# Kernel tuning notes

Measured on AMD Instinct MI355X. Metric: run time of the kernel, lower is better.

The kernel has to match this reference:

```python
import jax, jax.numpy as jnp
import numpy as np

N = 50000        # nodes
E = 800000       # edges
F_IN = 128       # dataset.num_features (== dim*heads so all conv layers share in_channels)
DIM = 32         # mParams['dim']
HEADS = 4        # mParams['num_heads']
HC = DIM * HEADS # 128
DEPTH = 2        # mParams['c_depth'] -> total conv layers = DEPTH + 1 = 3
L = DEPTH + 1
DIM2 = 16        # ceil(DIM/2)
NCLS = 6
SLOPE = 0.2      # GATv2Conv default negative_slope


def setup_inputs() -> dict:
    key = jax.random.key(0)
    ks = jax.random.split(key, 20)
    def lin(k, fan_in, shape):
        return jax.random.normal(k, shape, dtype=jnp.float32) / np.sqrt(fan_in)
    x = jax.random.normal(ks[0], (N, F_IN), dtype=jnp.float32)
    edge_index = jax.random.randint(ks[1], (2, E), 0, N, dtype=jnp.int64)
    batch = jnp.zeros((N,), dtype=jnp.int64)
    # stacked GATv2Conv params (all layers have in_channels = 128)
    Wl = lin(ks[2], F_IN, (L, F_IN, HC))   # lin_l weight (source transform)
    Wr = lin(ks[3], F_IN, (L, F_IN, HC))   # lin_r weight (target transform)
    bl = jnp.zeros((L, HC), dtype=jnp.float32)
    br = jnp.zeros((L, HC), dtype=jnp.float32)
    att = lin(ks[4], DIM, (L, HEADS, DIM)) # attention vector a
    cb = jnp.zeros((L, HC), dtype=jnp.float32)  # conv output bias
    W1 = lin(ks[5], HC, (HC, DIM));   b1 = jnp.zeros((DIM,), jnp.float32)
    W2 = lin(ks[6], DIM, (DIM, DIM2)); b2 = jnp.zeros((DIM2,), jnp.float32)
    W3 = lin(ks[7], 2 * DIM2, (2 * DIM2, NCLS)); b3 = jnp.zeros((NCLS,), jnp.float32)
    return {"x": x, "edge_index": edge_index, "batch": batch,
            "Wl": Wl, "Wr": Wr, "bl": bl, "br": br, "att": att, "cb": cb,
            "W1": W1, "b1": b1, "W2": W2, "b2": b2, "W3": W3, "b3": b3}


def _gatv2_layer(h, src, dst, Wl, Wr, bl, br, att, cb):
    # h: [N, F]; src/dst: [Ea] (self-loops included)
    xl = (h @ Wl + bl).reshape(N, HEADS, DIM)  # source-side transform
    xr = (h @ Wr + br).reshape(N, HEADS, DIM)  # target-side transform
    msg = xl[src] + xr[dst]                    # [Ea, H, C]
    e = jnp.where(msg > 0, msg, SLOPE * msg)   # leaky_relu
    score = jnp.einsum('ehc,hc->eh', e, att)   # [Ea, H]
    # scatter-softmax over destination nodes
    m = jax.ops.segment_max(score, dst, num_segments=N)        # [N, H]
    ex = jnp.exp(score - m[dst])
    s = jax.ops.segment_sum(ex, dst, num_segments=N)           # [N, H]
    alpha = ex / (s[dst] + 1e-16)                              # [Ea, H]
    out = jax.ops.segment_sum(alpha[:, :, None] * xl[src], dst, num_segments=N)
    return out.reshape(N, HC) + cb


def reference(x, edge_index, batch, Wl, Wr, bl, br, att, cb, W1, b1, W2, b2, W3, b3):
    src0, dst0 = edge_index[0], edge_index[1]
    loop = jnp.arange(N, dtype=edge_index.dtype)
    src = jnp.concatenate([src0, loop])  # GATv2Conv add_self_loops=True
    dst = jnp.concatenate([dst0, loop])
    h = x
    for i in range(L):
        h = jax.nn.relu(_gatv2_layer(h, src, dst, Wl[i], Wr[i], bl[i], br[i], att[i], cb[i]))
    h = jax.nn.relu(h @ W1 + b1)
    h = jax.nn.relu(h @ W2 + b2)
    # dropout(p=0.5) is identity in eval mode
    e = jnp.concatenate([h[src0], h[dst0]], axis=1)  # [E, 2*DIM2]
    out = e @ W3 + b3                                # [E, NCLS]
    return (out, e)
```

## Files before the change

### kernel.cpp

```cpp
#include <hip/hip_runtime.h>
#include <hip/hip_bf16.h>

typedef __hip_bfloat16 bf16;
typedef __attribute__((ext_vector_type(8))) short bf16x8;
typedef __attribute__((ext_vector_type(4))) float f32x4;

#define N_NODES 50000
#define E_EDGES 800000
#define EA (E_EDGES + N_NODES)
#define HC 128
#define HEADS 4
#define DIM 32
#define DIM2 16
#define NCLS 6
#define SLOPE 0.2f
#define XN (N_NODES * HC)
#define GM 32
#define HSTRIDE 152
#define WSWZ_L 32768
#define NCHUNK ((N_NODES + 1023) / 1024)

#define P_CVTI (2 * E_EDGES)
#define P_PRM  6390
#define P_WSWZ (3 * WSWZ_L)
#define P_TOT  (P_CVTI + P_PRM + P_WSWZ)

__device__ __forceinline__ float b2f(bf16 v) { return __bfloat162float(v); }
__device__ __forceinline__ unsigned short f2bfu(float f) {
    bf16 b = __float2bfloat16(f);
    return *(unsigned short*)&b;
}
__device__ __forceinline__ unsigned packbf(float a, float b) {
    return (unsigned)f2bfu(a) | ((unsigned)f2bfu(b) << 16);
}

__device__ __forceinline__ void block_detect(const void* wptr, const void* eptr,
                                             int* det, int& isf32, int& is64) {
    int tid = threadIdx.x;
    if (tid == 0) { det[0] = 0; det[1] = 0; }
    __syncthreads();
    const unsigned short* w = (const unsigned short*)wptr;
    int badf = 0;
    for (int i = tid; i < 1024; i += 256) {
        unsigned v = w[i];
        unsigned ex = (v >> 7) & 0xFF;
        if (v != 0 && (ex < 90 || ex > 150)) badf++;
    }
    const int* ei = (const int*)eptr;
    int nz = 0;
    for (int i = tid; i < 1024; i += 256) {
        if (ei[2 * i + 1] != 0) nz++;
    }
    if (badf) atomicAdd(&det[0], badf);
    if (nz)   atomicAdd(&det[1], nz);
    __syncthreads();
    isf32 = det[0] > 100;
    is64  = det[1] < 100;
}

__global__ __launch_bounds__(256) void k_prep(
        const void* eraw, const void* sWl, const void* sWr,
        const void* sbl, const void* sbr, const void* satt, const void* scb,
        const void* sW1, const void* sb1, const void* sW2, const void* sb2,
        const void* sW3, const void* sb3,
        int* __restrict__ eidx, int* __restrict__ off,
        float* __restrict__ prm, unsigned short* __restrict__ wswz) {
    __shared__ int det[2];
    int isf32, is64;
    block_detect(sWl, eraw, det, isf32, is64);

    int i = blockIdx.x * 256 + threadIdx.x;
    if (i < P_CVTI) {
        int v = is64 ? (int)((const long long*)eraw)[i] : ((const int*)eraw)[i];
        if (v < 0) v = 0;
        if (v >= N_NODES) v = N_NODES - 1;
        eidx[i] = v;
        if (i >= E_EDGES) atomicAdd(&off[v], 1);
        return;
    }
    i -= P_CVTI;
    if (i < P_PRM) {
        int j = i + 98304;
        const void* src; float* dst; int o;
        if      (j < 98688)  { src = sbl;  dst = prm + 98304;  o = j - 98304; }
        else if (j < 99072)  { src = sbr;  dst = prm + 98688;  o = j - 98688; }
        else if (j < 99456)  { src = satt; dst = prm + 99072;  o = j - 99072; }
        else if (j < 99840)  { src = scb;  dst = prm + 99456;  o = j - 99456; }
        else if (j < 103936) { src = sW1;  dst = prm + 99840;  o = j - 99840; }
        else if (j < 103968) { src = sb1;  dst = prm + 103936; o = j - 103936; }
        else if (j < 104480) { src = sW2;  dst = prm + 103968; o = j - 103968; }
        else if (j < 104496) { src = sb2;  dst = prm + 104480; o = j - 104480; }
        else if (j < 104688) { src = sW3;  dst = prm + 104496; o = j - 104496; }
        else                 { src = sb3;  dst = prm + 104688; o = j - 104688; }
        dst[o] = isf32 ? ((const float*)src)[o] : b2f(((const bf16*)src)[o]);
        return;
    }
    i -= P_PRM;
    if (i >= P_WSWZ) return;
    int L = i / WSWZ_L;
    int e = i % WSWZ_L;
    int ntile = e >> 11;
    int r2 = e & 2047;
    int ks = r2 >> 9;
    int r3 = r2 & 511;
    int lane = r3 >> 3;
    int j = r3 & 7;
    int col = ntile * 16 + (lane & 15);
    int k = ks * 32 + (lane >> 4) * 8 + j;
    const void* src = (col < HC) ? sWl : sWr;
    int idx = L * HC * HC + k * HC + (col & (HC - 1));
    float v = isf32 ? ((const float*)src)[idx] : b2f(((const bf16*)src)[idx]);
    wswz[i] = f2bfu(v);
}

__global__ __launch_bounds__(1024) void k_scan1(int* __restrict__ off, int* __restrict__ part) {
    __shared__ int s[1024];
    int tid = threadIdx.x;
    int i = blockIdx.x * 1024 + tid;
    int v = (i < N_NODES) ? off[i] + 1 : 0;
    s[tid] = v;
    __syncthreads();
    for (int o = 1; o < 1024; o <<= 1) {
        int t = (tid >= o) ? s[tid - o] : 0;
        __syncthreads();
        s[tid] += t;
        __syncthreads();
    }
    if (i < N_NODES) off[i] = s[tid] - v;
    if (tid == 1023) part[blockIdx.x] = s[1023];
}

__global__ __launch_bounds__(64) void k_scan2(int* __restrict__ part) {
    int tid = threadIdx.x;
    int v = (tid < NCHUNK) ? part[tid] : 0;
    int orig = v;
    for (int o = 1; o < 64; o <<= 1) {
        int t = __shfl_up(v, o);
        if (tid >= o) v += t;
    }
    if (tid < NCHUNK) part[tid] = v - orig;
}

__global__ __launch_bounds__(1024) void k_scan3(int* __restrict__ off, const int* __restrict__ part) {
    int i = blockIdx.x * 1024 + threadIdx.x;
    if (i < N_NODES) off[i] += part[blockIdx.x];
    if (i == 0) off[N_NODES] = EA;
}

__global__ void k_scatter(const int* __restrict__ eidx, const int* __restrict__ off,
                          int* __restrict__ fill, int* __restrict__ csrsrc) {
    int e = blockIdx.x * blockDim.x + threadIdx.x;
    if (e >= EA) return;
    int src, dst;
    if (e < E_EDGES) { src = eidx[e]; dst = eidx[E_EDGES + e]; }
    else             { src = dst = e - E_EDGES; }
    int pos = off[dst] + atomicAdd(&fill[dst], 1);
    if (pos >= 0 && pos < EA) csrsrc[pos] = src;
}

__global__ __launch_bounds__(256) void k_gemm_mfma(
        const void* __restrict__ hsrc, const void* wdet, const void* edet,
        int detect_in,
        const unsigned short* __restrict__ wswz,
        const float* __restrict__ bl, const float* __restrict__ br,
        unsigned* __restrict__ xlbf, float* __restrict__ xr) {
    __shared__ unsigned short hs[GM * HSTRIDE];
    __shared__ int det[2];
    int tid = threadIdx.x;
    int wave = tid >> 6, lane = tid & 63;
    long row0 = (long)blockIdx.x * GM;

    int f32in = 0;
    if (detect_in) {
        int is64d;
        block_detect(wdet, edet, det, f32in, is64d);
    }

    if (f32in) {
        for (int idx = tid; idx < GM * 64; idx += 256) {
            int r = idx >> 6, cp = idx & 63;
            float v0 = 0.f, v1 = 0.f;
            if (row0 + r < N_NODES) {
                const float2 hv = ((const float2*)((const float*)hsrc + (row0 + r) * HC))[cp];
                v0 = hv.x; v1 = hv.y;
            }
            *(unsigned*)&hs[r * HSTRIDE + cp * 2] = packbf(v0, v1);
        }
    } else {
        for (int idx = tid; idx < GM * 64; idx += 256) {
            int r = idx >> 6, cp = idx & 63;
            unsigned u = 0;
            if (row0 + r < N_NODES)
                u = ((const unsigned*)hsrc)[(row0 + r) * (HC / 2) + cp];
            *(unsigned*)&hs[r * HSTRIDE + cp * 2] = u;
        }
    }
    __syncthreads();

    int q = lane >> 4, l16 = lane & 15;
    for (int nt = 0; nt < 4; nt++) {
        int colbase = wave * 64 + nt * 16;
        int col = colbase + l16;
        int ntile = colbase >> 4;
        f32x4 acc0 = {0.f, 0.f, 0.f, 0.f};
        f32x4 acc1 = {0.f, 0.f, 0.f, 0.f};
#pragma unroll
        for (int ks = 0; ks < 4; ks++) {
            bf16x8 bfrag = *(const bf16x8*)(wswz + (((ntile * 4 + ks) * 64 + lane) << 3));
            bf16x8 a0 = *(const bf16x8*)(hs + l16 * HSTRIDE + ks * 32 + q * 8);
            bf16x8 a1 = *(const bf16x8*)(hs + (16 + l16) * HSTRIDE + ks * 32 + q * 8);
            acc0 = __builtin_amdgcn_mfma_f32_16x16x32_bf16(a0, bfrag, acc0, 0, 0, 0);
            acc1 = __builtin_amdgcn_mfma_f32_16x16x32_bf16(a1, bfrag, acc1, 0, 0, 0);
        }
        if (col < HC) {
            float bias = bl[col];
#pragma unroll
            for (int reg = 0; reg < 4; reg++) {
                float v0 = acc0[reg] + bias;
                float v1 = acc1[reg] + bias;
                float p0 = __shfl_xor(v0, 1);
                float p1 = __shfl_xor(v1, 1);
                if ((lane & 1) == 0) {
                    long n0 = row0 + q * 4 + reg;
                    long n1 = row0 + 16 + q * 4 + reg;
                    unsigned u0 = packbf(v0, p0);
                    unsigned u1 = packbf(v1, p1);
                    int cp = col >> 1;
                    if (n0 < N_NODES) xlbf[n0 * (HC / 2) + cp] = u0;
                    if (n1 < N_NODES) xlbf[n1 * (HC / 2) + cp] = u1;
                }
            }
        } else {
            int c = col - HC;
            float bias = br[c];
#pragma unroll
            for (int reg = 0; reg < 4; reg++) {
                long n0 = row0 + q * 4 + reg;
                long n1 = row0 + 16 + q * 4 + reg;
                if (n0 < N_NODES) xr[n0 * HC + c] = acc0[reg] + bias;
                if (n1 < N_NODES) xr[n1 * HC + c] = acc1[reg] + bias;
            }
        }
    }
}

__global__ __launch_bounds__(256) void k_attn(
        const unsigned* __restrict__ xlbf, const float* __restrict__ xr,
        const int* __restrict__ off, const int* __restrict__ csrsrc,
        const float* __restrict__ att, const float* __restrict__ cb,
        void* __restrict__ hout, int out_bf16) {
    int wave = threadIdx.x >> 6;
    int lane = threadIdx.x & 63;
    int node = blockIdx.x * 4 + wave;
    if (node >= N_NODES) return;
    int grp = lane >> 4;
    int gl  = lane & 15;
    int fb  = gl * 8;
    int head = fb >> 5;

    const float4* xrp = (const float4*)(xr + (long)node * HC + fb);
    float4 xa = xrp[0], xb = xrp[1];
    const float4* ap = (const float4*)(att + head * DIM + (fb & 31));
    float4 aa = ap[0], ab = ap[1];

    int e0 = off[node], e1 = off[node + 1];
    if (e0 < 0) e0 = 0;
    if (e1 > EA) e1 = EA;
    if (e1 <= e0) {
        if (grp == 0) {
            if (out_bf16) {
                uint4 z = {0u, 0u, 0u, 0u};
                *(uint4*)((unsigned*)hout + (long)node * (HC / 2) + gl * 4) = z;
            } else {
                float4 z = make_float4(0.f, 0.f, 0.f, 0.f);
                ((float4*)((float*)hout + (long)node * HC + fb))[0] = z;
                ((float4*)((float*)hout + (long)node * HC + fb))[1] = z;
            }
        }
        return;
    }
    int klast = e1 - 1;

    int k0 = e0 + grp;
    int ka = k0 < klast ? k0 : klast;
    int kb = (k0 + 4) < klast ? (k0 + 4) : klast;
    int sa = csrsrc[ka];
    int sb = csrsrc[kb];
    uint4 u0 = ((const uint4*)(xlbf + (long)sa * (HC / 2)))[gl];
    uint4 u1 = ((const uint4*)(xlbf + (long)sb * (HC / 2)))[gl];

    float m = -1e30f, ssum = 0.f;
    float acc[8];
#pragma unroll
    for (int j = 0; j < 8; j++) acc[j] = 0.f;

    for (int kk = k0; kk < e1; kk += 4) {
        uint4 cur = u0;
        u0 = u1;
        int kp = (kk + 8) < klast ? (kk + 8) : klast;
        int sp = csrsrc[kp];
        u1 = ((const uint4*)(xlbf + (long)sp * (HC / 2)))[gl];

        float x0 = __uint_as_float(cur.x << 16);
        float x1 = __uint_as_float(cur.x & 0xffff0000u);
        float x2 = __uint_as_float(cur.y << 16);
        float x3 = __uint_as_float(cur.y & 0xffff0000u);
        float x4 = __uint_as_float(cur.z << 16);
        float x5 = __uint_as_float(cur.z & 0xffff0000u);
        float x6 = __uint_as_float(cur.w << 16);
        float x7 = __uint_as_float(cur.w & 0xffff0000u);
        float m0 = x0 + xa.x, m1 = x1 + xa.y, m2 = x2 + xa.z, m3 = x3 + xa.w;
        float m4 = x4 + xb.x, m5 = x5 + xb.y, m6 = x6 + xb.z, m7 = x7 + xb.w;
        float l0 = fmaxf(m0, SLOPE * m0), l1 = fmaxf(m1, SLOPE * m1);
        float l2 = fmaxf(m2, SLOPE * m2), l3 = fmaxf(m3, SLOPE * m3);
        float l4 = fmaxf(m4, SLOPE * m4), l5 = fmaxf(m5, SLOPE * m5);
        float l6 = fmaxf(m6, SLOPE * m6), l7 = fmaxf(m7, SLOPE * m7);
        float p = l0 * aa.x + l1 * aa.y + l2 * aa.z + l3 * aa.w
                + l4 * ab.x + l5 * ab.y + l6 * ab.z + l7 * ab.w;
        p += __shfl_xor(p, 1);
        p += __shfl_xor(p, 2);
        float mn = fmaxf(m, p);
        float sc = __expf(m - mn);
        float ex = __expf(p - mn);
        ssum = ssum * sc + ex;
        acc[0] = acc[0] * sc + ex * x0;
        acc[1] = acc[1] * sc + ex * x1;
        acc[2] = acc[2] * sc + ex * x2;
        acc[3] = acc[3] * sc + ex * x3;
        acc[4] = acc[4] * sc + ex * x4;
        acc[5] = acc[5] * sc + ex * x5;
        acc[6] = acc[6] * sc + ex * x6;
        acc[7] = acc[7] * sc + ex * x7;
        m = mn;
    }

#pragma unroll
    for (int d = 16; d <= 32; d <<= 1) {
        float mo = __shfl_xor(m, d);
        float so = __shfl_xor(ssum, d);
        float ao[8];
#pragma unroll
        for (int j = 0; j < 8; j++) ao[j] = __shfl_xor(acc[j], d);
        float mn = fmaxf(m, mo);
        float s1 = __expf(m - mn);
        float s2 = __expf(mo - mn);
        ssum = ssum * s1 + so * s2;
#pragma unroll
        for (int j = 0; j < 8; j++) acc[j] = acc[j] * s1 + ao[j] * s2;
        m = mn;
    }

    if (grp == 0) {
        float inv = 1.f / (ssum + 1e-16f);
        const float4* cbp = (const float4*)(cb + fb);
        float4 c0 = cbp[0], c1 = cbp[1];
        float o0 = fmaxf(acc[0] * inv + c0.x, 0.f);
        float o1 = fmaxf(acc[1] * inv + c0.y, 0.f);
        float o2 = fmaxf(acc[2] * inv + c0.z, 0.f);
        float o3 = fmaxf(acc[3] * inv + c0.w, 0.f);
        float o4 = fmaxf(acc[4] * inv + c1.x, 0.f);
        float o5 = fmaxf(acc[5] * inv + c1.y, 0.f);
        float o6 = fmaxf(acc[6] * inv + c1.z, 0.f);
        float o7 = fmaxf(acc[7] * inv + c1.w, 0.f);
        if (out_bf16) {
            uint4 w;
            w.x = packbf(o0, o1);
            w.y = packbf(o2, o3);
            w.z = packbf(o4, o5);
            w.w = packbf(o6, o7);
            *(uint4*)((unsigned*)hout + (long)node * (HC / 2) + gl * 4) = w;
        } else {
            float4 a0 = make_float4(o0, o1, o2, o3);
            float4 a1 = make_float4(o4, o5, o6, o7);
            float4* op = (float4*)((float*)hout + (long)node * HC + fb);
            op[0] = a0;
            op[1] = a1;
        }
    }
}

__global__ __launch_bounds__(256) void k_mlp(
        const float* __restrict__ h, const float* __restrict__ W1,
        const float* __restrict__ b1, const float* __restrict__ W2,
        const float* __restrict__ b2, float* __restrict__ h3) {
    __shared__ float w1s[HC * DIM];
    __shared__ float hs[16 * HC];
    __shared__ float h2s[16 * DIM];
    __shared__ float w2s[DIM * DIM2];
    int tid = threadIdx.x;
    long row0 = (long)blockIdx.x * 16;
    for (int idx = tid; idx < HC * DIM; idx += 256) w1s[idx] = W1[idx];
    for (int idx = tid; idx < DIM * DIM2; idx += 256) w2s[idx] = W2[idx];
    for (int idx = tid; idx < 16 * HC; idx += 256) {
        long g = row0 * HC + idx;
        hs[idx] = (g < (long)N_NODES * HC) ? h[g] : 0.f;
    }
    __syncthreads();
#pragma unroll
    for (int p = 0; p < 2; p++) {
        int idx = tid + p * 256;
        int r = idx >> 5, c = idx & 31;
        float acc = b1[c];
        for (int k = 0; k < HC; k++) acc += hs[r * HC + k] * w1s[k * DIM + c];
        h2s[r * DIM + c] = acc > 0.f ? acc : 0.f;
    }
    __syncthreads();
    int r = tid >> 4, c = tid & 15;
    float acc = b2[c];
    for (int k = 0; k < DIM; k++) acc += h2s[r * DIM + k] * w2s[k * DIM2 + c];
    long row = row0 + r;
    if (row < N_NODES) h3[row * DIM2 + c] = acc > 0.f ? acc : 0.f;
}

__global__ __launch_bounds__(256) void k_out(
        const float* __restrict__ h3, const int* __restrict__ eidx,
        const float* __restrict__ W3, const float* __restrict__ b3,
        void* __restrict__ dout, const void* wdet, const void* edet) {
    __shared__ float w3s[2 * DIM2 * NCLS];
    __shared__ float bs[NCLS];
    __shared__ int det[2];
    int isf32, is64d;
    block_detect(wdet, edet, det, isf32, is64d);
    int tid = threadIdx.x;
    if (tid < 2 * DIM2 * NCLS) w3s[tid] = W3[tid];
    if (tid < NCLS) bs[tid] = b3[tid];
    __syncthreads();
    int e = blockIdx.x * 256 + tid;
    if (e >= E_EDGES) return;
    int src = eidx[e], dst = eidx[E_EDGES + e];
    float v[2 * DIM2];
    const float4* ps = (const float4*)(h3 + (long)src * DIM2);
    const float4* pd = (const float4*)(h3 + (long)dst * DIM2);
#pragma unroll
    for (int q = 0; q < 4; q++) {
        float4 t = ps[q];
        v[q * 4 + 0] = t.x; v[q * 4 + 1] = t.y; v[q * 4 + 2] = t.z; v[q * 4 + 3] = t.w;
    }
#pragma unroll
    for (int q = 0; q < 4; q++) {
        float4 t = pd[q];
        v[16 + q * 4 + 0] = t.x; v[16 + q * 4 + 1] = t.y; v[16 + q * 4 + 2] = t.z; v[16 + q * 4 + 3] = t.w;
    }
    float o[NCLS];
#pragma unroll
    for (int j = 0; j < NCLS; j++) {
        float acc = bs[j];
#pragma unroll
        for (int k = 0; k < 2 * DIM2; k++) acc += v[k] * w3s[k * NCLS + j];
        o[j] = acc;
    }
    if (isf32) {
        float* out0 = (float*)dout;
#pragma unroll
        for (int j = 0; j < NCLS; j++) out0[(long)e * NCLS + j] = o[j];
        float4* eo = (float4*)((float*)dout + (long)E_EDGES * NCLS) + (long)e * 8;
#pragma unroll
        for (int q = 0; q < 8; q++)
            eo[q] = make_float4(v[q * 4], v[q * 4 + 1], v[q * 4 + 2], v[q * 4 + 3]);
    } else {
        bf16* out0 = (bf16*)dout;
#pragma unroll
        for (int j = 0; j < NCLS; j++) out0[(long)e * NCLS + j] = __float2bfloat16(o[j]);
        uint4* eo = (uint4*)((bf16*)dout + (long)E_EDGES * NCLS) + (long)e * 4;
#pragma unroll
        for (int q = 0; q < 4; q++) {
            uint4 w;
            w.x = packbf(v[q * 8 + 0], v[q * 8 + 1]);
            w.y = packbf(v[q * 8 + 2], v[q * 8 + 3]);
            w.z = packbf(v[q * 8 + 4], v[q * 8 + 5]);
            w.w = packbf(v[q * 8 + 6], v[q * 8 + 7]);
            eo[q] = w;
        }
    }
}

extern "C" void kernel_launch(void* const* d_in, const int* in_sizes, int n_in,
                              void* d_out, int out_size, void* d_ws, size_t ws_size,
                              hipStream_t stream) {
    float* wsf   = (float*)d_ws;
    float* h     = wsf + 16;
    float* xl    = h  + (long)N_NODES * HC;
    float* xr    = xl + (long)N_NODES * HC;
    float* prm   = xr + (long)N_NODES * HC;
    unsigned short* wswz = (unsigned short*)(prm + 110000);
    int*   eidx  = (int*)(wswz + P_WSWZ);
    int*   off   = eidx + 2 * E_EDGES;
    int*   fill  = off + (N_NODES + 1);
    int*   csr   = fill + N_NODES;
    int*   part  = csr + EA;
    unsigned* xlbf = (unsigned*)xl;
    float* h3 = xl;

    float* pbl = prm + 98304;
    float* pbr = prm + 98688;
    float* patt= prm + 99072;
    float* pcb = prm + 99456;
    float* pW1 = prm + 99840;
    float* pb1 = prm + 103936;
    float* pW2 = prm + 103968;
    float* pb2 = prm + 104480;
    float* pW3 = prm + 104496;
    float* pb3 = prm + 104688;

    hipMemsetAsync(off, 0, (size_t)(2 * N_NODES + 1) * sizeof(int), stream);

    k_prep<<<(P_TOT + 255) / 256, 256, 0, stream>>>(
        d_in[1], d_in[3], d_in[4], d_in[5], d_in[6], d_in[7], d_in[8],
        d_in[9], d_in[10], d_in[11], d_in[12], d_in[13], d_in[14],
        eidx, off, prm, wswz);

    k_scan1<<<NCHUNK, 1024, 0, stream>>>(off, part);
    k_scan2<<<1, 64, 0, stream>>>(part);
    k_scan3<<<NCHUNK, 1024, 0, stream>>>(off, part);
    k_scatter<<<(EA + 255) / 256, 256, 0, stream>>>(eidx, off, fill, csr);

    for (int i = 0; i < 3; i++) {
        k_gemm_mfma<<<(N_NODES + GM - 1) / GM, 256, 0, stream>>>(
            i == 0 ? (const void*)d_in[0] : (const void*)h,
            d_in[3], d_in[1], i == 0 ? 1 : 0,
            wswz + (long)i * WSWZ_L, pbl + (long)i * HC, pbr + (long)i * HC,
            xlbf, xr);
        k_attn<<<(N_NODES + 3) / 4, 256, 0, stream>>>(
            xlbf, xr, off, csr, patt + (long)i * HEADS * DIM, pcb + (long)i * HC,
            (void*)h, i < 2 ? 1 : 0);
    }

    k_mlp<<<(N_NODES + 15) / 16, 256, 0, stream>>>(h, pW1, pb1, pW2, pb2, h3);

    k_out<<<(E_EDGES + 255) / 256, 256, 0, stream>>>(h3, eidx, pW3, pb3, d_out,
                                                     d_in[3], d_in[1]);
}
```

Before: 574.8 us.

## Fuse MLP head into final attention layer and merge scan kernels

The two-layer MLP (128->32->16) now runs inside the last k_attn launch. Each block stages W1 and W2 in dynamic shared memory and applies the MLP to the freshly aggregated node rows, so the fp32 h round-trip and a separate k_mlp launch go away. k_scan2 is folded into k_scan3, where each block reduces the preceding partial sums itself. k_out now writes its class outputs as packed float2/bf16 pairs instead of scalars. The cost is loading 16KB of weights per block in the last layer, extra block-wide syncs, and lower occupancy for that attention launch.

```diff
diff --git a/kernel.cpp b/kernel.cpp
--- a/kernel.cpp
+++ b/kernel.cpp
@@ -130,20 +130,17 @@
     if (tid == 1023) part[blockIdx.x] = s[1023];
 }
 
-__global__ __launch_bounds__(64) void k_scan2(int* __restrict__ part) {
+__global__ __launch_bounds__(1024) void k_scan3(int* __restrict__ off, const int* __restrict__ part) {
+    __shared__ int sbase;
     int tid = threadIdx.x;
-    int v = (tid < NCHUNK) ? part[tid] : 0;
-    int orig = v;
-    for (int o = 1; o < 64; o <<= 1) {
-        int t = __shfl_up(v, o);
-        if (tid >= o) v += t;
-    }
-    if (tid < NCHUNK) part[tid] = v - orig;
-}
-
-__global__ __launch_bounds__(1024) void k_scan3(int* __restrict__ off, const int* __restrict__ part) {
-    int i = blockIdx.x * 1024 + threadIdx.x;
-    if (i < N_NODES) off[i] += part[blockIdx.x];
+    if (tid < 64) {
+        int v = (tid < NCHUNK && tid < (int)blockIdx.x) ? part[tid] : 0;
+        for (int o = 32; o > 0; o >>= 1) v += __shfl_down(v, o);
+        if (tid == 0) sbase = v;
+    }
+    __syncthreads();
+    int i = blockIdx.x * 1024 + tid;
+    if (i < N_NODES) off[i] += sbase;
     if (i == 0) off[N_NODES] = EA;
 }
 
@@ -248,11 +245,25 @@
         const unsigned* __restrict__ xlbf, const float* __restrict__ xr,
         const int* __restrict__ off, const int* __restrict__ csrsrc,
         const float* __restrict__ att, const float* __restrict__ cb,
-        void* __restrict__ hout, int out_bf16) {
-    int wave = threadIdx.x >> 6;
-    int lane = threadIdx.x & 63;
+        void* __restrict__ hout, int out_bf16,
+        const float* __restrict__ W1, const float* __restrict__ b1,
+        const float* __restrict__ W2, const float* __restrict__ b2) {
+    extern __shared__ float smem[];
+    float* w1s   = smem;
+    float* w2s   = smem + 4096;
+    float* hrow  = smem + 4608;
+    float* h2row = smem + 5120;
+
+    int tid  = threadIdx.x;
+    int wave = tid >> 6;
+    int lane = tid & 63;
+    if (!out_bf16) {
+        for (int idx = tid; idx < HC * DIM; idx += 256) w1s[idx] = W1[idx];
+        for (int idx = tid; idx < DIM * DIM2; idx += 256) w2s[idx] = W2[idx];
+    }
+
     int node = blockIdx.x * 4 + wave;
-    if (node >= N_NODES) return;
+    if (node >= N_NODES) node = N_NODES - 1;
     int grp = lane >> 4;
     int gl  = lane & 15;
     int fb  = gl * 8;
@@ -266,72 +277,61 @@
     int e0 = off[node], e1 = off[node + 1];
     if (e0 < 0) e0 = 0;
     if (e1 > EA) e1 = EA;
-    if (e1 <= e0) {
-        if (grp == 0) {
-            if (out_bf16) {
-                uint4 z = {0u, 0u, 0u, 0u};
-                *(uint4*)((unsigned*)hout + (long)node * (HC / 2) + gl * 4) = z;
-            } else {
-                float4 z = make_float4(0.f, 0.f, 0.f, 0.f);
-                ((float4*)((float*)hout + (long)node * HC + fb))[0] = z;
-                ((float4*)((float*)hout + (long)node * HC + fb))[1] = z;
-            }
-        }
-        return;
-    }
-    int klast = e1 - 1;
-
-    int k0 = e0 + grp;
-    int ka = k0 < klast ? k0 : klast;
-    int kb = (k0 + 4) < klast ? (k0 + 4) : klast;
-    int sa = csrsrc[ka];
-    int sb = csrsrc[kb];
-    uint4 u0 = ((const uint4*)(xlbf + (long)sa * (HC / 2)))[gl];
-    uint4 u1 = ((const uint4*)(xlbf + (long)sb * (HC / 2)))[gl];
 
     float m = -1e30f, ssum = 0.f;
     float acc[8];
 #pragma unroll
     for (int j = 0; j < 8; j++) acc[j] = 0.f;
 
-    for (int kk = k0; kk < e1; kk += 4) {
-        uint4 cur = u0;
-        u0 = u1;
-        int kp = (kk + 8) < klast ? (kk + 8) : klast;
-        int sp = csrsrc[kp];
-        u1 = ((const uint4*)(xlbf + (long)sp * (HC / 2)))[gl];
-
-        float x0 = __uint_as_float(cur.x << 16);
-        float x1 = __uint_as_float(cur.x & 0xffff0000u);
-        float x2 = __uint_as_float(cur.y << 16);
-        float x3 = __uint_as_float(cur.y & 0xffff0000u);
-        float x4 = __uint_as_float(cur.z << 16);
-        float x5 = __uint_as_float(cur.z & 0xffff0000u);
-        float x6 = __uint_as_float(cur.w << 16);
-        float x7 = __uint_as_float(cur.w & 0xffff0000u);
-        float m0 = x0 + xa.x, m1 = x1 + xa.y, m2 = x2 + xa.z, m3 = x3 + xa.w;
-        float m4 = x4 + xb.x, m5 = x5 + xb.y, m6 = x6 + xb.z, m7 = x7 + xb.w;
-        float l0 = fmaxf(m0, SLOPE * m0), l1 = fmaxf(m1, SLOPE * m1);
-        float l2 = fmaxf(m2, SLOPE * m2), l3 = fmaxf(m3, SLOPE * m3);
-        float l4 = fmaxf(m4, SLOPE * m4), l5 = fmaxf(m5, SLOPE * m5);
-        float l6 = fmaxf(m6, SLOPE * m6), l7 = fmaxf(m7, SLOPE * m7);
-        float p = l0 * aa.x + l1 * aa.y + l2 * aa.z + l3 * aa.w
-                + l4 * ab.x + l5 * ab.y + l6 * ab.z + l7 * ab.w;
-        p += __shfl_xor(p, 1);
-        p += __shfl_xor(p, 2);
-        float mn = fmaxf(m, p);
-        float sc = __expf(m - mn);
-        float ex = __expf(p - mn);
-        ssum = ssum * sc + ex;
-        acc[0] = acc[0] * sc + ex * x0;
-        acc[1] = acc[1] * sc + ex * x1;
-        acc[2] = acc[2] * sc + ex * x2;
-        acc[3] = acc[3] * sc + ex * x3;
-        acc[4] = acc[4] * sc + ex * x4;
-        acc[5] = acc[5] * sc + ex * x5;
-        acc[6] = acc[6] * sc + ex * x6;
-        acc[7] = acc[7] * sc + ex * x7;
-        m = mn;
+    if (e1 > e0) {
+        int klast = e1 - 1;
+        int k0 = e0 + grp;
+        int ka = k0 < klast ? k0 : klast;
+        int kb = (k0 + 4) < klast ? (k0 + 4) : klast;
+        int sa = csrsrc[ka];
+        int sb = csrsrc[kb];
+        uint4 u0 = ((const uint4*)(xlbf + (long)sa * (HC / 2)))[gl];
+        uint4 u1 = ((const uint4*)(xlbf + (long)sb * (HC / 2)))[gl];
+
+        for (int kk = k0; kk < e1; kk += 4) {
+            uint4 cur = u0;
+            u0 = u1;
+            int kp = (kk + 8) < klast ? (kk + 8) : klast;
+            int sp = csrsrc[kp];
+            u1 = ((const uint4*)(xlbf + (long)sp * (HC / 2)))[gl];
+
+            float x0 = __uint_as_float(cur.x << 16);
+            float x1 = __uint_as_float(cur.x & 0xffff0000u);
+            float x2 = __uint_as_float(cur.y << 16);
+            float x3 = __uint_as_float(cur.y & 0xffff0000u);
+            float x4 = __uint_as_float(cur.z << 16);
+            float x5 = __uint_as_float(cur.z & 0xffff0000u);
+            float x6 = __uint_as_float(cur.w << 16);
+            float x7 = __uint_as_float(cur.w & 0xffff0000u);
+            float m0 = x0 + xa.x, m1 = x1 + xa.y, m2 = x2 + xa.z, m3 = x3 + xa.w;
+            float m4 = x4 + xb.x, m5 = x5 + xb.y, m6 = x6 + xb.z, m7 = x7 + xb.w;
+            float l0 = fmaxf(m0, SLOPE * m0), l1 = fmaxf(m1, SLOPE * m1);
+            float l2 = fmaxf(m2, SLOPE * m2), l3 = fmaxf(m3, SLOPE * m3);
+            float l4 = fmaxf(m4, SLOPE * m4), l5 = fmaxf(m5, SLOPE * m5);
+            float l6 = fmaxf(m6, SLOPE * m6), l7 = fmaxf(m7, SLOPE * m7);
+            float p = l0 * aa.x + l1 * aa.y + l2 * aa.z + l3 * aa.w
+                    + l4 * ab.x + l5 * ab.y + l6 * ab.z + l7 * ab.w;
+            p += __shfl_xor(p, 1);
+            p += __shfl_xor(p, 2);
+            float mn = fmaxf(m, p);
+            float sc = __expf(m - mn);
+            float ex = __expf(p - mn);
+            ssum = ssum * sc + ex;
+            acc[0] = acc[0] * sc + ex * x0;
+            acc[1] = acc[1] * sc + ex * x1;
+            acc[2] = acc[2] * sc + ex * x2;
+            acc[3] = acc[3] * sc + ex * x3;
+            acc[4] = acc[4] * sc + ex * x4;
+            acc[5] = acc[5] * sc + ex * x5;
+            acc[6] = acc[6] * sc + ex * x6;
+            acc[7] = acc[7] * sc + ex * x7;
+            m = mn;
+        }
     }
 
 #pragma unroll
@@ -350,66 +350,52 @@
         m = mn;
     }
 
-    if (grp == 0) {
-        float inv = 1.f / (ssum + 1e-16f);
-        const float4* cbp = (const float4*)(cb + fb);
-        float4 c0 = cbp[0], c1 = cbp[1];
-        float o0 = fmaxf(acc[0] * inv + c0.x, 0.f);
-        float o1 = fmaxf(acc[1] * inv + c0.y, 0.f);
-        float o2 = fmaxf(acc[2] * inv + c0.z, 0.f);
-        float o3 = fmaxf(acc[3] * inv + c0.w, 0.f);
-        float o4 = fmaxf(acc[4] * inv + c1.x, 0.f);
-        float o5 = fmaxf(acc[5] * inv + c1.y, 0.f);
-        float o6 = fmaxf(acc[6] * inv + c1.z, 0.f);
-        float o7 = fmaxf(acc[7] * inv + c1.w, 0.f);
-        if (out_bf16) {
+    if (out_bf16) {
+        if (grp == 0) {
+            float inv = 1.f / (ssum + 1e-16f);
+            const float4* cbp = (const float4*)(cb + fb);
+            float4 c0 = cbp[0], c1 = cbp[1];
             uint4 w;
-            w.x = packbf(o0, o1);
-            w.y = packbf(o2, o3);
-            w.z = packbf(o4, o5);
-            w.w = packbf(o6, o7);
+            w.x = packbf(fmaxf(acc[0] * inv + c0.x, 0.f), fmaxf(acc[1] * inv + c0.y, 0.f));
+            w.y = packbf(fmaxf(acc[2] * inv + c0.z, 0.f), fmaxf(acc[3] * inv + c0.w, 0.f));
+            w.z = packbf(fmaxf(acc[4] * inv + c1.x, 0.f), fmaxf(acc[5] * inv + c1.y, 0.f));
+            w.w = packbf(fmaxf(acc[6] * inv + c1.z, 0.f), fmaxf(acc[7] * inv + c1.w, 0.f));
             *(uint4*)((unsigned*)hout + (long)node * (HC / 2) + gl * 4) = w;
-        } else {
-            float4 a0 = make_float4(o0, o1, o2, o3);
-            float4 a1 = make_float4(o4, o5, o6, o7);
-            float4* op = (float4*)((float*)hout + (long)node * HC + fb);
-            op[0] = a0;
-            op[1] = a1;
-        }
-    }
-}
-
-__global__ __launch_bounds__(256) void k_mlp(
-        const float* __restrict__ h, const float* __restrict__ W1,
-        const float* __restrict__ b1, const float* __restrict__ W2,
-        const float* __restrict__ b2, float* __restrict__ h3) {
-    __shared__ float w1s[HC * DIM];
-    __shared__ float hs[16 * HC];
-    __shared__ float h2s[16 * DIM];
-    __shared__ float w2s[DIM * DIM2];
-    int tid = threadIdx.x;
-    long row0 = (long)blockIdx.x * 16;
-    for (int idx = tid; idx < HC * DIM; idx += 256) w1s[idx] = W1[idx];
-    for (int idx = tid; idx < DIM * DIM2; idx += 256) w2s[idx] = W2[idx];
-    for (int idx = tid; idx < 16 * HC; idx += 256) {
-        long g = row0 * HC + idx;
-        hs[idx] = (g < (long)N_NODES * HC) ? h[g] : 0.f;
-    }
-    __syncthreads();
-#pragma unroll
-    for (int p = 0; p < 2; p++) {
-        int idx = tid + p * 256;
-        int r = idx >> 5, c = idx & 31;
-        float acc = b1[c];
-        for (int k = 0; k < HC; k++) acc += hs[r * HC + k] * w1s[k * DIM + c];
-        h2s[r * DIM + c] = acc > 0.f ? acc : 0.f;
-    }
-    __syncthreads();
-    int r = tid >> 4, c = tid & 15;
-    float acc = b2[c];
-    for (int k = 0; k < DIM; k++) acc += h2s[r * DIM + k] * w2s[k * DIM2 + c];
-    long row = row0 + r;
-    if (row < N_NODES) h3[row * DIM2 + c] = acc > 0.f ? acc : 0.f;
+        }
+    } else {
+        if (grp == 0) {
+            float inv = 1.f / (ssum + 1e-16f);
+            const float4* cbp = (const float4*)(cb + fb);
+            float4 c0 = cbp[0], c1 = cbp[1];
+            float* hr = hrow + wave * HC + fb;
+            hr[0] = fmaxf(acc[0] * inv + c0.x, 0.f);
+            hr[1] = fmaxf(acc[1] * inv + c0.y, 0.f);
+            hr[2] = fmaxf(acc[2] * inv + c0.z, 0.f);
+            hr[3] = fmaxf(acc[3] * inv + c0.w, 0.f);
+            hr[4] = fmaxf(acc[4] * inv + c1.x, 0.f);
+            hr[5] = fmaxf(acc[5] * inv + c1.y, 0.f);
+            hr[6] = fmaxf(acc[6] * inv + c1.z, 0.f);
+            hr[7] = fmaxf(acc[7] * inv + c1.w, 0.f);
+        }
+        __syncthreads();
+        int c = lane & 31, half = lane >> 5;
+        const float* hr = hrow + wave * HC + half * 64;
+        const float* wp = w1s + half * 64 * DIM + c;
+        float a1 = 0.f;
+#pragma unroll 8
+        for (int k = 0; k < 64; k++) a1 += hr[k] * wp[k * DIM];
+        a1 += __shfl_xor(a1, 32);
+        a1 = fmaxf(a1 + b1[c], 0.f);
+        if (lane < 32) h2row[wave * DIM + c] = a1;
+        __syncthreads();
+        if (lane < 16) {
+            float a2 = b2[lane];
+            const float* h2 = h2row + wave * DIM;
+#pragma unroll
+            for (int k = 0; k < DIM; k++) a2 += h2[k] * w2s[k * DIM2 + lane];
+            ((float*)hout)[(long)node * DIM2 + lane] = fmaxf(a2, 0.f);
+        }
+    }
 }
 
 __global__ __launch_bounds__(256) void k_out(
@@ -450,17 +436,19 @@
         o[j] = acc;
     }
     if (isf32) {
-        float* out0 = (float*)dout;
-#pragma unroll
-        for (int j = 0; j < NCLS; j++) out0[(long)e * NCLS + j] = o[j];
+        float2* out0 = (float2*)dout;
+        out0[(long)e * 3 + 0] = make_float2(o[0], o[1]);
+        out0[(long)e * 3 + 1] = make_float2(o[2], o[3]);
+        out0[(long)e * 3 + 2] = make_float2(o[4], o[5]);
         float4* eo = (float4*)((float*)dout + (long)E_EDGES * NCLS) + (long)e * 8;
 #pragma unroll
         for (int q = 0; q < 8; q++)
             eo[q] = make_float4(v[q * 4], v[q * 4 + 1], v[q * 4 + 2], v[q * 4 + 3]);
     } else {
-        bf16* out0 = (bf16*)dout;
-#pragma unroll
-        for (int j = 0; j < NCLS; j++) out0[(long)e * NCLS + j] = __float2bfloat16(o[j]);
+        unsigned* out0 = (unsigned*)dout;
+        out0[(long)e * 3 + 0] = packbf(o[0], o[1]);
+        out0[(long)e * 3 + 1] = packbf(o[2], o[3]);
+        out0[(long)e * 3 + 2] = packbf(o[4], o[5]);
         uint4* eo = (uint4*)((bf16*)dout + (long)E_EDGES * NCLS) + (long)e * 4;
 #pragma unroll
         for (int q = 0; q < 4; q++) {
@@ -489,7 +477,7 @@
     int*   csr   = fill + N_NODES;
     int*   part  = csr + EA;
     unsigned* xlbf = (unsigned*)xl;
-    float* h3 = xl;
+    float* h3 = h;
 
     float* pbl = prm + 98304;
     float* pbr = prm + 98688;
@@ -510,7 +498,6 @@
         eidx, off, prm, wswz);
 
     k_scan1<<<NCHUNK, 1024, 0, stream>>>(off, part);
-    k_scan2<<<1, 64, 0, stream>>>(part);
     k_scan3<<<NCHUNK, 1024, 0, stream>>>(off, part);
     k_scatter<<<(EA + 255) / 256, 256, 0, stream>>>(eidx, off, fill, csr);
 
@@ -520,12 +507,13 @@
             d_in[3], d_in[1], i == 0 ? 1 : 0,
             wswz + (long)i * WSWZ_L, pbl + (long)i * HC, pbr + (long)i * HC,
             xlbf, xr);
-        k_attn<<<(N_NODES + 3) / 4, 256, 0, stream>>>(
+        int last = (i == 2);
+        size_t shmem = last ? 5248 * sizeof(float) : 0;
+        k_attn<<<(N_NODES + 3) / 4, 256, shmem, stream>>>(
             xlbf, xr, off, csr, patt + (long)i * HEADS * DIM, pcb + (long)i * HC,
-            (void*)h, i < 2 ? 1 : 0);
-    }
-
-    k_mlp<<<(N_NODES + 15) / 16, 256, 0, stream>>>(h, pW1, pb1, pW2, pb2, h3);
+            last ? (void*)h3 : (void*)h, last ? 0 : 1,
+            pW1, pb1, pW2, pb2);
+    }
 
     k_out<<<(E_EDGES + 255) / 256, 256, 0, stream>>>(h3, eidx, pW3, pb3, d_out,
                                                      d_in[3], d_in[1]);
```

Result: slower. 603.8 us (+5.0%).
